# Optimization experiments

Measured on AMD Instinct MI355X. Metric: run time of the kernel, lower is better.

The kernel has to match this reference:

```python
import jax, jax.numpy as jnp
import numpy as np
import math

HIDDEN = 1024
HEADS = 16
HEAD_DIM = HIDDEN // HEADS
B, S = 4, 2048


def setup_inputs() -> dict:
    key = jax.random.key(0)
    ks = jax.random.split(key, 10)
    x = jax.random.normal(ks[0], (B, S, HIDDEN), dtype=jnp.float32)
    time_intervals = jax.random.uniform(ks[1], (B, S, S), dtype=jnp.float32)
    mask = jax.random.randint(ks[2], (B, 1, S, S), 0, 2, dtype=jnp.int32)
    scale = 1.0 / math.sqrt(HIDDEN)
    Wq = jax.random.normal(ks[3], (HIDDEN, HIDDEN), dtype=jnp.float32) * scale
    bq = jnp.zeros((HIDDEN,), dtype=jnp.float32)
    Wk = jax.random.normal(ks[4], (HIDDEN, HIDDEN), dtype=jnp.float32) * scale
    bk = jnp.zeros((HIDDEN,), dtype=jnp.float32)
    Wv = jax.random.normal(ks[5], (HIDDEN, HIDDEN), dtype=jnp.float32) * scale
    bv = jnp.zeros((HIDDEN,), dtype=jnp.float32)
    alpha = jnp.asarray(0.1, dtype=jnp.float32)
    return {"x": x, "time_intervals": time_intervals, "mask": mask,
            "Wq": Wq, "bq": bq, "Wk": Wk, "bk": bk, "Wv": Wv, "bv": bv,
            "alpha": alpha}


def reference(x, time_intervals, mask, Wq, bq, Wk, bk, Wv, bv, alpha):
    b, s, _ = x.shape
    # projections -> [b, heads, s, head_dim]
    def proj(W, bias):
        y = x @ W + bias
        return y.reshape(b, s, HEADS, HEAD_DIM).transpose(0, 2, 1, 3)
    Q = proj(Wq, bq)
    K = proj(Wk, bk)
    V = proj(Wv, bv)
    scores = jnp.einsum('bhqd,bhkd->bhqk', Q, K) / math.sqrt(HEAD_DIM)
    # additive time-decay bias, broadcast over heads
    scores = scores + (-jnp.abs(alpha)) * time_intervals[:, None, :, :]
    scores = jnp.where(mask == 0, jnp.float32(-1e9), scores)
    attn = jax.nn.softmax(scores, axis=-1)
    out = jnp.einsum('bhqk,bhkd->bhqd', attn, V)
    return out.transpose(0, 2, 1, 3).reshape(b, s, HIDDEN)
```

## Files before the change

kernel.cpp:

```cpp
#include <hip/hip_runtime.h>
#include <hip/hip_bf16.h>
#include <hip/hip_fp16.h>

#define BATCH 4
#define SEQ   2048
#define HID   1024
#define HEADS 16
#define HDIM  64
#define MROWS (BATCH * SEQ)
#define LOG2E 1.4426950408889634f
#define SCL   (LOG2E / 8.0f)

typedef _Float16 v8h __attribute__((ext_vector_type(8)));
typedef _Float16 v4h __attribute__((ext_vector_type(4)));
typedef _Float16 v2h __attribute__((ext_vector_type(2)));
typedef float    v4f __attribute__((ext_vector_type(4)));
typedef int      v4i __attribute__((ext_vector_type(4)));

#define MFMA16(a, b, c) __builtin_amdgcn_mfma_f32_16x16x32_f16((a), (b), (c), 0, 0, 0)
#define MFMA16K16(a, b, c) __builtin_amdgcn_mfma_f32_16x16x16f16((a), (b), (c), 0, 0, 0)

__device__ inline int pk2(float a, float b) {
    return __builtin_bit_cast(int, __builtin_amdgcn_cvt_pkrtz(a, b));
}

__device__ __forceinline__ void async16(const void* g, void* l) {
    __builtin_amdgcn_global_load_lds(
        (const __attribute__((address_space(1))) unsigned int*)g,
        (__attribute__((address_space(3))) unsigned int*)l, 16, 0, 0);
}

#define SWZ(row, chunk) (((row) * 64) + ((((chunk) ^ ((row) & 7))) * 8))

__global__ __launch_bounds__(256) void cvt_x(const float* __restrict__ x,
                                             _Float16* __restrict__ xb) {
    int i = blockIdx.x * 256 + threadIdx.x;
    const float4* xp = (const float4*)x;
    float4 a = xp[2 * i];
    float4 b = xp[2 * i + 1];
    v4i o;
    o[0] = pk2(a.x, a.y); o[1] = pk2(a.z, a.w);
    o[2] = pk2(b.x, b.y); o[3] = pk2(b.z, b.w);
    ((v4i*)xb)[i] = o;
}

__global__ __launch_bounds__(256) void transw(const float* __restrict__ W0,
                                              const float* __restrict__ W1,
                                              const float* __restrict__ W2,
                                              _Float16* __restrict__ Wt) {
    const float* W = (blockIdx.z == 0) ? W0 : (blockIdx.z == 1 ? W1 : W2);
    _Float16* dst = Wt + (size_t)blockIdx.z * HID * HID;
    __shared__ float t[32][33];
    int bx = blockIdx.x * 32, by = blockIdx.y * 32;
    int tx = threadIdx.x, ty = threadIdx.y;
#pragma unroll
    for (int i = 0; i < 4; i++)
        t[ty + i * 8][tx] = W[(size_t)(by + ty + i * 8) * HID + bx + tx];
    __syncthreads();
#pragma unroll
    for (int i = 0; i < 4; i++)
        dst[(size_t)(bx + ty + i * 8) * HID + by + tx] = (_Float16)t[tx][ty + i * 8];
}

__global__ __launch_bounds__(256) void mkbias(const float* __restrict__ tiv,
                                              const int* __restrict__ msk,
                                              const float* __restrict__ alphap,
                                              _Float16* __restrict__ biasT) {
    __shared__ _Float16 L[16 * 264];
    const int b = blockIdx.z, Q16 = blockIdx.y, kc0 = blockIdx.x * 256;
    const int tid = threadIdx.x;
    const float ca = -fabsf(alphap[0]) * LOG2E;
    const int prow = tid >> 6;
    const int pcol = (tid & 63) * 4;
#pragma unroll
    for (int pi = 0; pi < 4; pi++) {
        int r = pi * 4 + prow;
        size_t g = ((size_t)b * SEQ + Q16 * 16 + r) * SEQ + kc0 + pcol;
        float4 tv = *(const float4*)(tiv + g);
        int4   mv = *(const int4*)(msk + g);
        float f0 = mv.x ? ca * tv.x : -57344.0f;
        float f1 = mv.y ? ca * tv.y : -57344.0f;
        float f2 = mv.z ? ca * tv.z : -57344.0f;
        float f3 = mv.w ? ca * tv.w : -57344.0f;
        int2 o; o.x = pk2(f0, f1); o.y = pk2(f2, f3);
        *(int2*)&L[r * 264 + pcol] = o;
    }
    __syncthreads();
    const int lane = tid & 63, tq = tid >> 6;
#pragma unroll
    for (int it = 0; it < 4; it++) {
        int K16i = it * 4 + tq;
        int kl = K16i * 16 + (lane >> 4) * 4;
        int qr = lane & 15;
        int2 v = *(const int2*)&L[qr * 264 + kl];
        size_t o = ((((size_t)b * 128 + (kc0 >> 4) + K16i) * 128 + Q16) * 64 + lane) * 4;
        *(int2*)&biasT[o] = v;
    }
}

__global__ __launch_bounds__(256) void gemm_qkv(
    const _Float16* __restrict__ xb, const _Float16* __restrict__ wt,
    const float* __restrict__ bq, const float* __restrict__ bk,
    const float* __restrict__ bv,
    _Float16* __restrict__ Qb, _Float16* __restrict__ Kb, _Float16* __restrict__ Vtb) {
    const int mode = blockIdx.z;
    const _Float16* w = wt + (size_t)mode * HID * HID;
    __shared__ _Float16 As[128 * 64];
    __shared__ _Float16 Bs[128 * 64];
    const int tid = threadIdx.x;
    const int wv = tid >> 6, lane = tid & 63;
    const int quad = lane >> 4, l15 = lane & 15;
    const int wr = wv >> 1, wc = wv & 1;
    const int m0 = blockIdx.y * 128;
    const int n0 = blockIdx.x * 128;

    v4f acc[4][4];
#pragma unroll
    for (int i = 0; i < 4; i++)
#pragma unroll
        for (int j = 0; j < 4; j++) acc[i][j] = (v4f){0.f, 0.f, 0.f, 0.f};

    const int srow = lane >> 3;
    const int schk = lane & 7;
    const _Float16* Ag = xb + (size_t)m0 * HID;
    const _Float16* Bg = w + (size_t)n0 * HID;

    for (int k0 = 0; k0 < HID; k0 += 64) {
        __syncthreads();
#pragma unroll
        for (int i = 0; i < 4; i++) {
            int ra = wv * 32 + i * 8 + srow;
            int ca = schk ^ (ra & 7);
            async16(Ag + (size_t)ra * HID + k0 + ca * 8, &As[(wv * 32 + i * 8) * 64]);
            async16(Bg + (size_t)ra * HID + k0 + ca * 8, &Bs[(wv * 32 + i * 8) * 64]);
        }
        __syncthreads();
#pragma unroll
        for (int kc = 0; kc < 2; kc++) {
            v8h af[4], bf[4];
#pragma unroll
            for (int t = 0; t < 4; t++) {
                af[t] = *(const v8h*)&As[SWZ(wr * 64 + t * 16 + l15, kc * 4 + quad)];
                bf[t] = *(const v8h*)&Bs[SWZ(wc * 64 + t * 16 + l15, kc * 4 + quad)];
            }
#pragma unroll
            for (int tm = 0; tm < 4; tm++)
#pragma unroll
                for (int tn = 0; tn < 4; tn++)
                    acc[tm][tn] = MFMA16(af[tm], bf[tn], acc[tm][tn]);
        }
    }

    const float* pb = (mode == 0) ? bq : (mode == 1 ? bk : bv);
    const float oscl = (mode == 0) ? SCL : 1.0f;
#pragma unroll
    for (int tm = 0; tm < 4; tm++) {
#pragma unroll
        for (int tn = 0; tn < 4; tn++) {
            int n = n0 + wc * 64 + tn * 16 + l15;
            float bval = pb[n];
            int h = n >> 6, d = n & 63;
#pragma unroll
            for (int r = 0; r < 4; r++) {
                int m = m0 + wr * 64 + tm * 16 + quad * 4 + r;
                int b = m >> 11, s = m & 2047;
                _Float16 hv = (_Float16)((acc[tm][tn][r] + bval) * oscl);
                if (mode == 2) {
                    Vtb[(((size_t)(b * HEADS + h) * HDIM + d) * SEQ) + s] = hv;
                } else {
                    _Float16* dst = (mode == 0) ? Qb : Kb;
                    dst[((size_t)(b * HEADS + h) * SEQ + s) * HDIM + d] = hv;
                }
            }
        }
    }
}

__global__ __launch_bounds__(256, 4) void attn(
    const _Float16* __restrict__ Qb, const _Float16* __restrict__ Kb,
    const _Float16* __restrict__ Vtb, const _Float16* __restrict__ biasT,
    float* __restrict__ out) {
    const int bh = blockIdx.y;
    const int b = bh >> 4, h = bh & 15;
    const int qt = blockIdx.x;
    const int tid = threadIdx.x;
    const int wv = tid >> 6, lane = tid & 63;
    const int quad = lane >> 4, l15 = lane & 15;

    __shared__ _Float16 Ks[64 * 64];
    __shared__ _Float16 Vs[64 * 64];

    const int q0 = qt * 128 + wv * 32;
    const int Q16a = q0 >> 4;

    const _Float16* Qp = Qb + (size_t)(b * HEADS + h) * SEQ * HDIM;
    const _Float16* Kp = Kb + (size_t)(b * HEADS + h) * SEQ * HDIM;
    const _Float16* Vp = Vtb + (size_t)(b * HEADS + h) * HDIM * SEQ;
    const _Float16* Bbase = biasT + (size_t)b * 128 * 128 * 64 * 4;

    v8h qf[2][2];
#pragma unroll
    for (int tm = 0; tm < 2; tm++)
#pragma unroll
        for (int kc = 0; kc < 2; kc++)
            qf[tm][kc] = *(const v8h*)&Qp[(size_t)(q0 + tm * 16 + l15) * HDIM + kc * 32 + quad * 8];

    v4f oacc[2][4];
#pragma unroll
    for (int i = 0; i < 2; i++)
#pragma unroll
        for (int j = 0; j < 4; j++) oacc[i][j] = (v4f){0.f, 0.f, 0.f, 0.f};
    float lsum[2] = {0.f, 0.f};

    const int srow = lane >> 3, schk = lane & 7;

    for (int kt = 0; kt < SEQ / 64; kt++) {
        const int key0 = kt * 64;
        v4f sacc[4][2];
#pragma unroll
        for (int nt = 0; nt < 4; nt++)
#pragma unroll
            for (int tm = 0; tm < 2; tm++) {
                int2 bl = *(const int2*)&Bbase[((((size_t)(key0 >> 4) + nt) * 128 + Q16a + tm) * 64 + lane) * 4];
                v4h bv = __builtin_bit_cast(v4h, bl);
                sacc[nt][tm] = (v4f){(float)bv[0], (float)bv[1], (float)bv[2], (float)bv[3]};
            }

        __syncthreads();
#pragma unroll
        for (int i = 0; i < 2; i++) {
            int r = wv * 16 + i * 8 + srow;
            int c = schk ^ (r & 7);
            async16(Kp + (size_t)(key0 + r) * HDIM + c * 8, &Ks[(wv * 16 + i * 8) * 64]);
            async16(Vp + (size_t)r * SEQ + key0 + c * 8, &Vs[(wv * 16 + i * 8) * 64]);
        }
        __syncthreads();

#pragma unroll
        for (int kc = 0; kc < 2; kc++) {
            v8h kfr[4];
#pragma unroll
            for (int nt = 0; nt < 4; nt++)
                kfr[nt] = *(const v8h*)&Ks[SWZ(nt * 16 + l15, kc * 4 + quad)];
#pragma unroll
            for (int nt = 0; nt < 4; nt++)
#pragma unroll
                for (int tm = 0; tm < 2; tm++)
                    sacc[nt][tm] = MFMA16(kfr[nt], qf[tm][kc], sacc[nt][tm]);
        }

        int2 pfr[4][2];
#pragma unroll
        for (int nt = 0; nt < 4; nt++)
#pragma unroll
            for (int tm = 0; tm < 2; tm++) {
                float p0 = __builtin_amdgcn_exp2f(sacc[nt][tm][0]);
                float p1 = __builtin_amdgcn_exp2f(sacc[nt][tm][1]);
                float p2 = __builtin_amdgcn_exp2f(sacc[nt][tm][2]);
                float p3 = __builtin_amdgcn_exp2f(sacc[nt][tm][3]);
                int2 pkv;
                pkv.x = pk2(p0, p1);
                pkv.y = pk2(p2, p3);
                lsum[tm] += (p0 + p1) + (p2 + p3);
                pfr[nt][tm] = pkv;
            }

#pragma unroll
        for (int g = 0; g < 4; g++) {
            v4h vfr[4];
#pragma unroll
            for (int nt = 0; nt < 4; nt++) {
                int row = nt * 16 + l15;
                int cc = g * 2 + (quad >> 1);
                vfr[nt] = *(const v4h*)&Vs[row * 64 + ((cc ^ (row & 7)) * 8) + (quad & 1) * 4];
            }
#pragma unroll
            for (int tm = 0; tm < 2; tm++) {
                v4h pa = __builtin_bit_cast(v4h, pfr[g][tm]);
#pragma unroll
                for (int nt = 0; nt < 4; nt++)
                    oacc[tm][nt] = MFMA16K16(pa, vfr[nt], oacc[tm][nt]);
            }
        }
    }

#pragma unroll
    for (int tm = 0; tm < 2; tm++) {
        float lt = lsum[tm];
        lt += __shfl_xor(lt, 16);
        lt += __shfl_xor(lt, 32);
        float inv[4];
#pragma unroll
        for (int r = 0; r < 4; r++)
            inv[r] = 1.0f / __shfl(lt, quad * 4 + r);
#pragma unroll
        for (int nt = 0; nt < 4; nt++)
#pragma unroll
            for (int r = 0; r < 4; r++) {
                int q = q0 + tm * 16 + quad * 4 + r;
                int d = nt * 16 + l15;
                out[((size_t)b * SEQ + q) * HID + h * HDIM + d] = oacc[tm][nt][r] * inv[r];
            }
    }
}

extern "C" void kernel_launch(void* const* d_in, const int* in_sizes, int n_in,
                              void* d_out, int out_size, void* d_ws, size_t ws_size,
                              hipStream_t stream) {
    const float* x    = (const float*)d_in[0];
    const float* tiv  = (const float*)d_in[1];
    const int*   msk  = (const int*)d_in[2];
    const float* Wq   = (const float*)d_in[3];
    const float* bq   = (const float*)d_in[4];
    const float* Wk   = (const float*)d_in[5];
    const float* bk   = (const float*)d_in[6];
    const float* Wv   = (const float*)d_in[7];
    const float* bv   = (const float*)d_in[8];
    const float* alp  = (const float*)d_in[9];

    char* ws = (char*)d_ws;
    const size_t XB_OFF = 0;
    const size_t WT_OFF = XB_OFF + (size_t)MROWS * HID * 2;
    const size_t Q_OFF  = WT_OFF + (size_t)3 * HID * HID * 2;
    const size_t K_OFF  = Q_OFF + (size_t)MROWS * HID * 2;
    const size_t V_OFF  = K_OFF + (size_t)MROWS * HID * 2;
    const size_t B_OFF  = V_OFF + (size_t)MROWS * HID * 2;

    _Float16* xb   = (_Float16*)(ws + XB_OFF);
    _Float16* wt   = (_Float16*)(ws + WT_OFF);
    _Float16* Qb   = (_Float16*)(ws + Q_OFF);
    _Float16* Kb   = (_Float16*)(ws + K_OFF);
    _Float16* Vtb  = (_Float16*)(ws + V_OFF);
    _Float16* bias = (_Float16*)(ws + B_OFF);

    cvt_x<<<MROWS * HID / (256 * 8), 256, 0, stream>>>(x, xb);
    dim3 tb(32, 8);
    transw<<<dim3(32, 32, 3), tb, 0, stream>>>(Wq, Wk, Wv, wt);
    mkbias<<<dim3(SEQ / 256, SEQ / 16, BATCH), 256, 0, stream>>>(tiv, msk, alp, bias);
    gemm_qkv<<<dim3(HID / 128, MROWS / 128, 3), 256, 0, stream>>>(
        xb, wt, bq, bk, bv, Qb, Kb, Vtb);
    attn<<<dim3(SEQ / 128, BATCH * HEADS), 256, 0, stream>>>(Qb, Kb, Vtb, bias,
                                                             (float*)d_out);
}
```

Before: 391.6 us.

## Double-buffer K/V shared tiles, prefetch bias, and remap attention workgroups

Adds a second shared-memory buffer for the K and V tiles so the next tile's async copies are issued before the current tile's MFMAs, leaving one barrier per iteration instead of two. The next tile's time-decay bias values are also loaded a step ahead into registers. Workgroup IDs are remapped so neighbouring blocks spread across (batch, head) groups, which changes cache and XCD locality. Shared memory per block doubles and register use rises, which may lower occupancy under the 4-blocks launch bound. Whether the async copies are guaranteed complete at the single end-of-iteration barrier depends on how async16 waits, which the visible code does not show.

```diff
diff --git a/kernel.cpp b/kernel.cpp
--- a/kernel.cpp
+++ b/kernel.cpp
@@ -180,15 +180,17 @@
     const _Float16* __restrict__ Qb, const _Float16* __restrict__ Kb,
     const _Float16* __restrict__ Vtb, const _Float16* __restrict__ biasT,
     float* __restrict__ out) {
-    const int bh = blockIdx.y;
+    const int wg  = (blockIdx.y << 4) | blockIdx.x;
+    const int nid = ((wg & 7) << 7) | (wg >> 3);
+    const int bh = nid >> 4;
+    const int qt = nid & 15;
     const int b = bh >> 4, h = bh & 15;
-    const int qt = blockIdx.x;
     const int tid = threadIdx.x;
     const int wv = tid >> 6, lane = tid & 63;
     const int quad = lane >> 4, l15 = lane & 15;
 
-    __shared__ _Float16 Ks[64 * 64];
-    __shared__ _Float16 Vs[64 * 64];
+    __shared__ _Float16 Ks[2][64 * 64];
+    __shared__ _Float16 Vs[2][64 * 64];
 
     const int q0 = qt * 128 + wv * 32;
     const int Q16a = q0 >> 4;
@@ -214,34 +216,57 @@
 
     const int srow = lane >> 3, schk = lane & 7;
 
+#define STAGE(buf_, key0_)                                                  \
+    {                                                                       \
+        _Pragma("unroll")                                                   \
+        for (int i_ = 0; i_ < 2; i_++) {                                    \
+            int r_ = wv * 16 + i_ * 8 + srow;                               \
+            int c_ = schk ^ (r_ & 7);                                       \
+            async16(Kp + (size_t)((key0_) + r_) * HDIM + c_ * 8,            \
+                    &Ks[buf_][(wv * 16 + i_ * 8) * 64]);                    \
+            async16(Vp + (size_t)r_ * SEQ + (key0_) + c_ * 8,               \
+                    &Vs[buf_][(wv * 16 + i_ * 8) * 64]);                    \
+        }                                                                   \
+    }
+
+#define BLOAD(key0_)                                                        \
+    {                                                                       \
+        _Pragma("unroll")                                                   \
+        for (int nt_ = 0; nt_ < 4; nt_++)                                   \
+            _Pragma("unroll")                                               \
+            for (int tm_ = 0; tm_ < 2; tm_++)                               \
+                bl[nt_][tm_] = *(const int2*)&Bbase[((((size_t)((key0_) >> 4) + nt_) * 128 + Q16a + tm_) * 64 + lane) * 4]; \
+    }
+
+    int2 bl[4][2];
+    STAGE(0, 0)
+    BLOAD(0)
+    __syncthreads();
+
     for (int kt = 0; kt < SEQ / 64; kt++) {
+        const int cur = kt & 1;
         const int key0 = kt * 64;
+
         v4f sacc[4][2];
 #pragma unroll
         for (int nt = 0; nt < 4; nt++)
 #pragma unroll
             for (int tm = 0; tm < 2; tm++) {
-                int2 bl = *(const int2*)&Bbase[((((size_t)(key0 >> 4) + nt) * 128 + Q16a + tm) * 64 + lane) * 4];
-                v4h bv = __builtin_bit_cast(v4h, bl);
+                v4h bv = __builtin_bit_cast(v4h, bl[nt][tm]);
                 sacc[nt][tm] = (v4f){(float)bv[0], (float)bv[1], (float)bv[2], (float)bv[3]};
             }
 
-        __syncthreads();
-#pragma unroll
-        for (int i = 0; i < 2; i++) {
-            int r = wv * 16 + i * 8 + srow;
-            int c = schk ^ (r & 7);
-            async16(Kp + (size_t)(key0 + r) * HDIM + c * 8, &Ks[(wv * 16 + i * 8) * 64]);
-            async16(Vp + (size_t)r * SEQ + key0 + c * 8, &Vs[(wv * 16 + i * 8) * 64]);
-        }
-        __syncthreads();
+        if (kt + 1 < SEQ / 64) {
+            STAGE(cur ^ 1, key0 + 64)
+            BLOAD(key0 + 64)
+        }
 
 #pragma unroll
         for (int kc = 0; kc < 2; kc++) {
             v8h kfr[4];
 #pragma unroll
             for (int nt = 0; nt < 4; nt++)
-                kfr[nt] = *(const v8h*)&Ks[SWZ(nt * 16 + l15, kc * 4 + quad)];
+                kfr[nt] = *(const v8h*)&Ks[cur][SWZ(nt * 16 + l15, kc * 4 + quad)];
 #pragma unroll
             for (int nt = 0; nt < 4; nt++)
 #pragma unroll
@@ -272,7 +297,7 @@
             for (int nt = 0; nt < 4; nt++) {
                 int row = nt * 16 + l15;
                 int cc = g * 2 + (quad >> 1);
-                vfr[nt] = *(const v4h*)&Vs[row * 64 + ((cc ^ (row & 7)) * 8) + (quad & 1) * 4];
+                vfr[nt] = *(const v4h*)&Vs[cur][row * 64 + ((cc ^ (row & 7)) * 8) + (quad & 1) * 4];
             }
 #pragma unroll
             for (int tm = 0; tm < 2; tm++) {
@@ -282,7 +307,12 @@
                     oacc[tm][nt] = MFMA16K16(pa, vfr[nt], oacc[tm][nt]);
             }
         }
-    }
+
+        __syncthreads();
+    }
+
+#undef STAGE
+#undef BLOAD
 
 #pragma unroll
     for (int tm = 0; tm < 2; tm++) {
```

Measured after the change: 392.9 us. Within noise of the previous version (+0.3%).
